# Optimization experiments

Hardware: AMD Instinct MI355X
Metric: run time of the kernel (lower is better)

Reference implementation:

```python
import jax, jax.numpy as jnp
import numpy as np

REPR_IN = (16, 16, 8)
REPR_OUT = (32, 16, 8)
NUM_BASIS = 16
MAX_RADIUS = 2.0
GAMMA = 16.0  # radial basis sharpness

def _dim(repr_):
    return sum(m * (2 * l + 1) for l, m in enumerate(repr_))

DIM_IN = _dim(REPR_IN)          # 104
SIZE_OUT = _dim(REPR_OUT)       # 120
NUM_GATES = sum(REPR_OUT[1:])   # 24
DIM_OUT = SIZE_OUT + NUM_GATES  # 144 (conv emits gates too)


def setup_inputs() -> dict:
    key = jax.random.key(0)
    k1, k2, k3, k4 = jax.random.split(key, 4)
    B, N, M = 4, 1024, 1024
    features = jax.random.normal(k1, (B, DIM_IN, M), jnp.float32)
    difference_matrix = jax.random.normal(k2, (B, N, M, 3), jnp.float32)
    relative_mask = jax.random.uniform(k3, (B, N, M), jnp.float32)
    W = jax.random.normal(k4, (NUM_BASIS, DIM_OUT, DIM_IN), jnp.float32) / np.sqrt(NUM_BASIS * DIM_IN)
    return {"features": features, "difference_matrix": difference_matrix,
            "relative_mask": relative_mask, "W": W}


def _radial_basis(diff):
    # diff: [B, N, M, 3] -> phi: [B, N, M, K]
    r = jnp.sqrt(jnp.sum(diff * diff, axis=-1) + 1e-12)
    centers = jnp.linspace(0.0, MAX_RADIUS, NUM_BASIS, dtype=diff.dtype)
    return jnp.exp(-GAMMA * jnp.square(r[..., None] - centers))


def reference(features, difference_matrix, relative_mask, W):
    # SE3PointConvolution: per-pair kernel K[b,n,m] = sum_k phi_k(|r_nm|) W[k]
    # masked by relative_mask; out[b,o,n] = sum_m K[b,n,m,o,i] feat[b,i,m].
    # Fused so the [B,N,M,144,104] kernel is never materialized.
    phi = _radial_basis(difference_matrix) * relative_mask[..., None]  # [B,N,M,K]
    tmp = jnp.einsum('bnmk,bim->bnki', phi, features)                  # [B,N,K,DIM_IN]
    y = jnp.einsum('bnki,koi->bon', tmp, W)                            # [B,DIM_OUT,N]

    B, _, N = y.shape
    # scalar (l=0) activation, bias=False
    outs = [jax.nn.relu(y[:, :REPR_OUT[0]])]
    # gates: last NUM_GATES channels, sigmoid
    g = jax.nn.sigmoid(y[:, SIZE_OUT:])
    begin_y, begin_g = REPR_OUT[0], 0
    for l, mul in enumerate(REPR_OUT):
        if l == 0 or mul == 0:
            continue
        d = 2 * l + 1
        fy = y[:, begin_y:begin_y + mul * d].reshape(B, mul, d, N)
        fg = g[:, begin_g:begin_g + mul].reshape(B, mul, 1, N)
        outs.append((fy * fg).reshape(B, mul * d, N))
        begin_y += mul * d
        begin_g += mul
    return jnp.concatenate(outs, axis=1)  # [B, SIZE_OUT, N]
```

## Files before the change

### kernel.cpp

```cpp
#include <hip/hip_runtime.h>


typedef __attribute__((ext_vector_type(4))) float f32x4;
typedef __attribute__((ext_vector_type(8))) short s16x8;

#define DI 104
#define DO 144
#define MT 64
#define TTST 1688
#define YST 9

#define W_ELEMS 239616
#define F_ELEMS 425984

#define OFF_PHI0 0
#define OFF_PHI1 16384
#define OFF_FEAT0 32768
#define OFF_FEAT1 47104
#define OFF_Y 61440
#define SMEM_TOTAL (61440 + 144*9*4)

__device__ __forceinline__ float fexp2(float x) {
#if __has_builtin(__builtin_amdgcn_exp2f)
    return __builtin_amdgcn_exp2f(x);
#else
    return exp2f(x);
#endif
}
__device__ __forceinline__ float flog2(float x) {
#if __has_builtin(__builtin_amdgcn_logf)
    return __builtin_amdgcn_logf(x);
#else
    return log2f(x);
#endif
}
__device__ __forceinline__ float fsqrt_(float x) {
#if __has_builtin(__builtin_amdgcn_sqrtf)
    return __builtin_amdgcn_sqrtf(x);
#else
    return sqrtf(x);
#endif
}
__device__ __forceinline__ float frcp_(float x) {
#if __has_builtin(__builtin_amdgcn_rcpf)
    return __builtin_amdgcn_rcpf(x);
#else
    return 1.0f / x;
#endif
}
__device__ __forceinline__ unsigned int pkbf(float lo, float hi) {
    unsigned int a = __builtin_bit_cast(unsigned int, lo) + 0x8000u;
    unsigned int b = __builtin_bit_cast(unsigned int, hi) + 0x8000u;
    return __builtin_amdgcn_perm(b, a, 0x07060302u);
}
__device__ __forceinline__ unsigned short f2b(float f) {
    return (unsigned short)((__builtin_bit_cast(unsigned int, f) + 0x8000u) >> 16);
}

__global__ __launch_bounds__(256, 8)
void cvt_kernel(const float* __restrict__ feat_g, const float* __restrict__ W_g,
                unsigned short* __restrict__ ws)
{
    int gid = blockIdx.x * 256 + threadIdx.x;
    const float* src;
    unsigned short* dst;
    if (gid < W_ELEMS/8) {
        src = W_g + gid*8;  dst = ws + gid*8;
    } else {
        int g2 = gid - W_ELEMS/8;
        src = feat_g + g2*8; dst = ws + W_ELEMS + g2*8;
    }
    f32x4 a = *(const f32x4*)src;
    f32x4 b = *(const f32x4*)(src + 4);
    unsigned int o[4] = { pkbf(a[0],a[1]), pkbf(a[2],a[3]), pkbf(b[0],b[1]), pkbf(b[2],b[3]) };
    *(f32x4*)dst = *(f32x4*)o;
}

__global__ __launch_bounds__(512, 4)
void pgb_kernel(const unsigned short* __restrict__ ws,
                const float* __restrict__ diff_g,
                const float* __restrict__ mask_g,
                float* __restrict__ out_g)
{
    const unsigned short* Wbf    = ws;
    const unsigned short* featbf = ws + W_ELEMS;

    __shared__ __align__(16) unsigned char smem[SMEM_TOTAL];
    unsigned short* Tt   = (unsigned short*)(smem);
    float*          ylds = (float*)(smem + OFF_Y);

    const int t    = threadIdx.x;
    const int b    = blockIdx.x >> 7;
    const int n0   = (blockIdx.x & 127) << 3;
    const int wave = t >> 6;
    const int lane = t & 63;
    const int l15  = lane & 15;
    const int q    = lane >> 4;
    const int wr   = wave >> 1;
    const int ct0  = (wave & 1) << 2;
    const int sw   = l15 & 7;

    if (t < 256) {
        ((unsigned int*)(smem + OFF_FEAT0 + DI*128))[t] = 0u;
        ((unsigned int*)(smem + OFF_FEAT1 + DI*128))[t] = 0u;
    }

    f32x4 acc[2][4];
#pragma unroll
    for (int rr = 0; rr < 2; ++rr)
#pragma unroll
        for (int cc = 0; cc < 4; ++cc)
            acc[rr][cc] = (f32x4){0.f, 0.f, 0.f, 0.f};

    const int pn = t >> 6;
    const int kh = (t >> 5) & 1;
    const int pml = (t & 31) << 1;
    const int pblk = (t & 31) >> 2;
    const int pin  = pml & 7;
    const float CEXP = -23.083120654223414f;
    const float A1   = 6.155498841126244f;
    const float V2   = -0.8207331788168325f;
    const float K0OFF = kh ? 1.0666666666666667f : 0.f;
    const float S0B   = kh ? -6.976232019943076f : -0.41036658940841624f;
    const size_t dmrow = (size_t)((b << 10) + n0 + pn) << 10;

    const int fi0 = t >> 3, fj = t & 7;
    const int fi1 = 64 + (t >> 3);
    const int fjs = (fj ^ (fi0 & 7)) << 3;
    const size_t fbase = (size_t)b * DI << 10;

    float dx0, dy0, dz0, dx1, dy1, dz1, mk0, mk1;
    s16x8 fr0 = {}, fr1 = {};
    {
        const float* dp = diff_g + (dmrow + pml)*3;
        dx0=dp[0]; dy0=dp[1]; dz0=dp[2]; dx1=dp[3]; dy1=dp[4]; dz1=dp[5];
        const float* mp = mask_g + dmrow + pml;
        mk0=mp[0]; mk1=mp[1];
        fr0 = *(const s16x8*)(featbf + fbase + ((size_t)fi0 << 10) + (fj << 3));
        if (t < 320)
            fr1 = *(const s16x8*)(featbf + fbase + ((size_t)fi1 << 10) + (fj << 3));
    }

    for (int s = 0; s < 16; ++s) {
        const int ms = s * MT;
        unsigned short* phibuf  = (unsigned short*)(smem + ((s & 1) ? OFF_PHI1 : OFF_PHI0));
        unsigned short* featbuf = (unsigned short*)(smem + ((s & 1) ? OFF_FEAT1 : OFF_FEAT0));
        {
            float r0 = fsqrt_(fmaf(dx0,dx0, fmaf(dy0,dy0, fmaf(dz0,dz0, 1e-12f))));
            float r1 = fsqrt_(fmaf(dx1,dx1, fmaf(dy1,dy1, fmaf(dz1,dz1, 1e-12f))));
            float t0 = r0 - K0OFF, t1 = r1 - K0OFF;
            float E0 = fmaf(CEXP*t0, t0, flog2(mk0));
            float E1 = fmaf(CEXP*t1, t1, flog2(mk1));
            float s0 = fmaf(A1, r0, S0B);
            float s1 = fmaf(A1, r1, S0B);
            unsigned short* pw = phibuf + (pn*16 + kh*8)*64 + pin;
#pragma unroll
            for (int j = 0; j < 8; ++j) {
                float p0 = fexp2(E0);
                float p1 = fexp2(E1);
                *(unsigned int*)(pw + j*64 + ((pblk ^ j) << 3)) = pkbf(p0, p1);
                E0 += s0; s0 += V2;
                E1 += s1; s1 += V2;
            }
        }
        *(s16x8*)(featbuf + fi0*64 + fjs) = fr0;
        if (t < 320)
            *(s16x8*)(featbuf + fi1*64 + fjs) = fr1;
        __syncthreads();
        if (s < 15) {
            const float* dp = diff_g + (dmrow + ms + MT + pml)*3;
            dx0=dp[0]; dy0=dp[1]; dz0=dp[2]; dx1=dp[3]; dy1=dp[4]; dz1=dp[5];
            const float* mp = mask_g + dmrow + ms + MT + pml;
            mk0=mp[0]; mk1=mp[1];
            fr0 = *(const s16x8*)(featbf + fbase + ((size_t)fi0 << 10) + ms + MT + (fj << 3));
            if (t < 320)
                fr1 = *(const s16x8*)(featbf + fbase + ((size_t)fi1 << 10) + ms + MT + (fj << 3));
        }
#pragma unroll
        for (int kk = 0; kk < 2; ++kk) {
            const int mo = ((kk*4 + q) ^ sw) << 3;
            s16x8 a0 = *(const s16x8*)(phibuf + ((2*wr    )*16 + l15)*64 + mo);
            s16x8 a1 = *(const s16x8*)(phibuf + ((2*wr + 1)*16 + l15)*64 + mo);
#pragma unroll
            for (int cc = 0; cc < 4; ++cc) {
                if (ct0 + cc < 7) {
                    s16x8 bf = *(const s16x8*)(featbuf + ((ct0+cc)*16 + l15)*64 + mo);
                    acc[0][cc] = __builtin_amdgcn_mfma_f32_16x16x32_bf16(a0, bf, acc[0][cc], 0, 0, 0);
                    acc[1][cc] = __builtin_amdgcn_mfma_f32_16x16x32_bf16(a1, bf, acc[1][cc], 0, 0, 0);
                }
            }
        }
    }

    __syncthreads();

#pragma unroll
    for (int rr = 0; rr < 2; ++rr) {
        int nloc = 2*wr + rr;
#pragma unroll
        for (int cc = 0; cc < 4; ++cc) {
            int i = (ct0+cc)*16 + l15;
            if (ct0 + cc < 7 && i < DI) {
#pragma unroll
                for (int r = 0; r < 4; ++r)
                    Tt[nloc*TTST + (q*4+r)*DI + i] = f2b(acc[rr][cc][r]);
            }
        }
    }
    __syncthreads();

    f32x4 y0 = (f32x4){0.f,0.f,0.f,0.f}, y1 = (f32x4){0.f,0.f,0.f,0.f};
    const int o0 = wave*16 + l15;
    const int o1 = 128 + l15;
#pragma unroll 4
    for (int s3 = 0; s3 < 52; ++s3) {
        int a = s3*4 + q;
        int k = a / 13;
        int i = (a - k*13) << 3;
        s16x8 bf = *(const s16x8*)(Tt + (l15 & 7)*TTST + s3*32 + q*8);
        s16x8 af = *(const s16x8*)(Wbf + (size_t)(k*DO + o0)*DI + i);
        y0 = __builtin_amdgcn_mfma_f32_16x16x32_bf16(af, bf, y0, 0, 0, 0);
        if (wave == 0) {
            s16x8 ag = *(const s16x8*)(Wbf + (size_t)(k*DO + o1)*DI + i);
            y1 = __builtin_amdgcn_mfma_f32_16x16x32_bf16(ag, bf, y1, 0, 0, 0);
        }
    }
    if (l15 < 8) {
#pragma unroll
        for (int r = 0; r < 4; ++r)
            ylds[(wave*16 + q*4 + r)*YST + l15] = y0[r];
        if (wave == 0) {
#pragma unroll
            for (int r = 0; r < 4; ++r)
                ylds[(128 + q*4 + r)*YST + l15] = y1[r];
        }
    }
    __syncthreads();

    const float L2E = 1.4426950408889634f;
    for (int idx = t; idx < 120*8; idx += 512) {
        int o = idx >> 3, nn = idx & 7;
        float y = ylds[o*YST + nn];
        float v;
        if (o < 32) {
            v = fmaxf(y, 0.f);
        } else if (o < 80) {
            float g = ylds[(120 + (o-32)/3)*YST + nn];
            v = y * frcp_(1.f + fexp2(-g*L2E));
        } else {
            float g = ylds[(136 + (o-80)/5)*YST + nn];
            v = y * frcp_(1.f + fexp2(-g*L2E));
        }
        out_g[((size_t)(b*120 + o) << 10) + n0 + nn] = v;
    }
}

extern "C" void kernel_launch(void* const* d_in, const int* in_sizes, int n_in,
                              void* d_out, int out_size, void* d_ws, size_t ws_size,
                              hipStream_t stream) {
    const float* feat = (const float*)d_in[0];
    const float* diff = (const float*)d_in[1];
    const float* mask = (const float*)d_in[2];
    const float* W    = (const float*)d_in[3];
    float* out = (float*)d_out;
    unsigned short* ws = (unsigned short*)d_ws;
    (void)in_sizes; (void)n_in; (void)out_size; (void)ws_size;
    cvt_kernel<<<dim3((W_ELEMS + F_ELEMS)/8/256), dim3(256), 0, stream>>>(feat, W, ws);
    pgb_kernel<<<dim3(512), dim3(512), 0, stream>>>(ws, diff, mask, out);
}
```

Baseline: 142.5 us.

## Compute radial basis in registers per wave and feed MFMA directly, drop LDS staging

Each wave now owns one output row n and computes phi for its own 16 basis functions and 8 m-values per lane directly in registers, packing them into the MFMA A operand. Features are loaded straight from global memory into B fragments instead of being staged through double-buffered LDS, which removes the per-step __syncthreads and the phi/feature LDS traffic. The diff/mask loads are vectorized and software-pipelined across half-steps, and the mask is multiplied in linear space instead of folded into the exponent via log2. The trade-off is redundant global feature loads across the 8 waves (relying on cache), more exp evaluations per lane, and higher register pressure.

After: 246.4 us. 1.73x slower.

```diff
diff --git a/kernel.cpp b/kernel.cpp
--- a/kernel.cpp
+++ b/kernel.cpp
@@ -3,35 +3,24 @@
 
 typedef __attribute__((ext_vector_type(4))) float f32x4;
 typedef __attribute__((ext_vector_type(8))) short s16x8;
+typedef __attribute__((ext_vector_type(4))) unsigned int u32x4;
 
 #define DI 104
 #define DO 144
-#define MT 64
 #define TTST 1688
 #define YST 9
 
 #define W_ELEMS 239616
 #define F_ELEMS 425984
 
-#define OFF_PHI0 0
-#define OFF_PHI1 16384
-#define OFF_FEAT0 32768
-#define OFF_FEAT1 47104
-#define OFF_Y 61440
-#define SMEM_TOTAL (61440 + 144*9*4)
+#define OFF_Y 27008
+#define SMEM_TOTAL (27008 + 144*9*4)
 
 __device__ __forceinline__ float fexp2(float x) {
 #if __has_builtin(__builtin_amdgcn_exp2f)
     return __builtin_amdgcn_exp2f(x);
 #else
     return exp2f(x);
-#endif
-}
-__device__ __forceinline__ float flog2(float x) {
-#if __has_builtin(__builtin_amdgcn_logf)
-    return __builtin_amdgcn_logf(x);
-#else
-    return log2f(x);
 #endif
 }
 __device__ __forceinline__ float fsqrt_(float x) {
@@ -86,7 +75,7 @@
     const unsigned short* featbf = ws + W_ELEMS;
 
     __shared__ __align__(16) unsigned char smem[SMEM_TOTAL];
-    unsigned short* Tt   = (unsigned short*)(smem);
+    unsigned short* Tt   = (unsigned short*)smem;
     float*          ylds = (float*)(smem + OFF_Y);
 
     const int t    = threadIdx.x;
@@ -96,115 +85,75 @@
     const int lane = t & 63;
     const int l15  = lane & 15;
     const int q    = lane >> 4;
-    const int wr   = wave >> 1;
-    const int ct0  = (wave & 1) << 2;
-    const int sw   = l15 & 7;
-
-    if (t < 256) {
-        ((unsigned int*)(smem + OFF_FEAT0 + DI*128))[t] = 0u;
-        ((unsigned int*)(smem + OFF_FEAT1 + DI*128))[t] = 0u;
-    }
-
-    f32x4 acc[2][4];
-#pragma unroll
-    for (int rr = 0; rr < 2; ++rr)
-#pragma unroll
-        for (int cc = 0; cc < 4; ++cc)
-            acc[rr][cc] = (f32x4){0.f, 0.f, 0.f, 0.f};
-
-    const int pn = t >> 6;
-    const int kh = (t >> 5) & 1;
-    const int pml = (t & 31) << 1;
-    const int pblk = (t & 31) >> 2;
-    const int pin  = pml & 7;
+    const int mq   = q << 3;
+
     const float CEXP = -23.083120654223414f;
-    const float A1   = 6.155498841126244f;
-    const float V2   = -0.8207331788168325f;
-    const float K0OFF = kh ? 1.0666666666666667f : 0.f;
-    const float S0B   = kh ? -6.976232019943076f : -0.41036658940841624f;
-    const size_t dmrow = (size_t)((b << 10) + n0 + pn) << 10;
-
-    const int fi0 = t >> 3, fj = t & 7;
-    const int fi1 = 64 + (t >> 3);
-    const int fjs = (fj ^ (fi0 & 7)) << 3;
-    const size_t fbase = (size_t)b * DI << 10;
-
-    float dx0, dy0, dz0, dx1, dy1, dz1, mk0, mk1;
-    s16x8 fr0 = {}, fr1 = {};
-    {
-        const float* dp = diff_g + (dmrow + pml)*3;
-        dx0=dp[0]; dy0=dp[1]; dz0=dp[2]; dx1=dp[3]; dy1=dp[4]; dz1=dp[5];
-        const float* mp = mask_g + dmrow + pml;
-        mk0=mp[0]; mk1=mp[1];
-        fr0 = *(const s16x8*)(featbf + fbase + ((size_t)fi0 << 10) + (fj << 3));
-        if (t < 320)
-            fr1 = *(const s16x8*)(featbf + fbase + ((size_t)fi1 << 10) + (fj << 3));
-    }
-
+    const float ck   = (float)l15 * (2.0f/15.0f);
+    const float B1k  = -2.0f * CEXP * ck;
+    const float B0k  = CEXP * ck * ck;
+
+    const size_t drow  = ((size_t)((b << 10) + n0 + wave)) << 10;
+    const size_t fbase = ((size_t)b * DI) << 10;
+
+    f32x4 acc[7];
+#pragma unroll
+    for (int cc = 0; cc < 7; ++cc) acc[cc] = (f32x4){0.f, 0.f, 0.f, 0.f};
+
+    f32x4 D0[6], D1[6], M0[2], M1[2];
+
+    auto loadDM = [&](f32x4* D, f32x4* M, int m0) {
+        const float* dp = diff_g + (drow + m0)*3;
+#pragma unroll
+        for (int u = 0; u < 6; ++u) D[u] = *(const f32x4*)(dp + 4*u);
+        const float* mp = mask_g + drow + m0;
+        M[0] = *(const f32x4*)mp;
+        M[1] = *(const f32x4*)(mp + 4);
+    };
+
+    auto halfstep = [&](const f32x4* D, const f32x4* M, int m0) {
+        s16x8 bfr[7];
+#pragma unroll
+        for (int cc = 0; cc < 6; ++cc) {
+            int i = cc*16 + l15;
+            bfr[cc] = *(const s16x8*)(featbf + fbase + ((size_t)i << 10) + m0);
+        }
+        bfr[6] = *(const s16x8*)(featbf + fbase + ((size_t)(96 + (l15 & 7)) << 10) + m0);
+        if (l15 >= 8) bfr[6] = (s16x8){0,0,0,0,0,0,0,0};
+        float p[8];
+#pragma unroll
+        for (int j = 0; j < 8; ++j) {
+            float dx = D[(3*j+0) >> 2][(3*j+0) & 3];
+            float dy = D[(3*j+1) >> 2][(3*j+1) & 3];
+            float dz = D[(3*j+2) >> 2][(3*j+2) & 3];
+            float r  = fsqrt_(fmaf(dx, dx, fmaf(dy, dy, fmaf(dz, dz, 1e-12f))));
+            float e  = fmaf(r, fmaf(CEXP, r, B1k), B0k);
+            p[j] = fexp2(e) * M[j >> 2][j & 3];
+        }
+        u32x4 pk;
+        pk[0] = pkbf(p[0], p[1]); pk[1] = pkbf(p[2], p[3]);
+        pk[2] = pkbf(p[4], p[5]); pk[3] = pkbf(p[6], p[7]);
+        s16x8 af = __builtin_bit_cast(s16x8, pk);
+#pragma unroll
+        for (int cc = 0; cc < 7; ++cc)
+            acc[cc] = __builtin_amdgcn_mfma_f32_16x16x32_bf16(af, bfr[cc], acc[cc], 0, 0, 0);
+    };
+
+    loadDM(D0, M0, mq);
     for (int s = 0; s < 16; ++s) {
-        const int ms = s * MT;
-        unsigned short* phibuf  = (unsigned short*)(smem + ((s & 1) ? OFF_PHI1 : OFF_PHI0));
-        unsigned short* featbuf = (unsigned short*)(smem + ((s & 1) ? OFF_FEAT1 : OFF_FEAT0));
-        {
-            float r0 = fsqrt_(fmaf(dx0,dx0, fmaf(dy0,dy0, fmaf(dz0,dz0, 1e-12f))));
-            float r1 = fsqrt_(fmaf(dx1,dx1, fmaf(dy1,dy1, fmaf(dz1,dz1, 1e-12f))));
-            float t0 = r0 - K0OFF, t1 = r1 - K0OFF;
-            float E0 = fmaf(CEXP*t0, t0, flog2(mk0));
-            float E1 = fmaf(CEXP*t1, t1, flog2(mk1));
-            float s0 = fmaf(A1, r0, S0B);
-            float s1 = fmaf(A1, r1, S0B);
-            unsigned short* pw = phibuf + (pn*16 + kh*8)*64 + pin;
-#pragma unroll
-            for (int j = 0; j < 8; ++j) {
-                float p0 = fexp2(E0);
-                float p1 = fexp2(E1);
-                *(unsigned int*)(pw + j*64 + ((pblk ^ j) << 3)) = pkbf(p0, p1);
-                E0 += s0; s0 += V2;
-                E1 += s1; s1 += V2;
-            }
-        }
-        *(s16x8*)(featbuf + fi0*64 + fjs) = fr0;
-        if (t < 320)
-            *(s16x8*)(featbuf + fi1*64 + fjs) = fr1;
-        __syncthreads();
-        if (s < 15) {
-            const float* dp = diff_g + (dmrow + ms + MT + pml)*3;
-            dx0=dp[0]; dy0=dp[1]; dz0=dp[2]; dx1=dp[3]; dy1=dp[4]; dz1=dp[5];
-            const float* mp = mask_g + dmrow + ms + MT + pml;
-            mk0=mp[0]; mk1=mp[1];
-            fr0 = *(const s16x8*)(featbf + fbase + ((size_t)fi0 << 10) + ms + MT + (fj << 3));
-            if (t < 320)
-                fr1 = *(const s16x8*)(featbf + fbase + ((size_t)fi1 << 10) + ms + MT + (fj << 3));
-        }
-#pragma unroll
-        for (int kk = 0; kk < 2; ++kk) {
-            const int mo = ((kk*4 + q) ^ sw) << 3;
-            s16x8 a0 = *(const s16x8*)(phibuf + ((2*wr    )*16 + l15)*64 + mo);
-            s16x8 a1 = *(const s16x8*)(phibuf + ((2*wr + 1)*16 + l15)*64 + mo);
-#pragma unroll
-            for (int cc = 0; cc < 4; ++cc) {
-                if (ct0 + cc < 7) {
-                    s16x8 bf = *(const s16x8*)(featbuf + ((ct0+cc)*16 + l15)*64 + mo);
-                    acc[0][cc] = __builtin_amdgcn_mfma_f32_16x16x32_bf16(a0, bf, acc[0][cc], 0, 0, 0);
-                    acc[1][cc] = __builtin_amdgcn_mfma_f32_16x16x32_bf16(a1, bf, acc[1][cc], 0, 0, 0);
-                }
-            }
-        }
-    }
-
-    __syncthreads();
-
-#pragma unroll
-    for (int rr = 0; rr < 2; ++rr) {
-        int nloc = 2*wr + rr;
-#pragma unroll
-        for (int cc = 0; cc < 4; ++cc) {
-            int i = (ct0+cc)*16 + l15;
-            if (ct0 + cc < 7 && i < DI) {
-#pragma unroll
-                for (int r = 0; r < 4; ++r)
-                    Tt[nloc*TTST + (q*4+r)*DI + i] = f2b(acc[rr][cc][r]);
-            }
+        const int m00 = s*64 + mq;
+        loadDM(D1, M1, m00 + 32);
+        halfstep(D0, M0, m00);
+        if (s < 15) loadDM(D0, M0, m00 + 64);
+        halfstep(D1, M1, m00 + 32);
+    }
+
+#pragma unroll
+    for (int cc = 0; cc < 7; ++cc) {
+        int i = cc*16 + l15;
+        if (cc < 6 || l15 < 8) {
+#pragma unroll
+            for (int r = 0; r < 4; ++r)
+                Tt[wave*TTST + (q*4 + r)*DI + i] = f2b(acc[cc][r]);
         }
     }
     __syncthreads();
```

## Software-pipeline phi generation one stage ahead of MFMA GEMM

Applied to the files above, without the earlier changes.

Restructures the main loop so the radial-basis phi tile and feature tile for stage s+1 are computed and written to the alternate LDS buffer while stage s is consumed by MFMA, with global loads prefetched two stages ahead. This leaves one barrier per iteration instead of a compute-then-sync-then-GEMM sequence, letting exp/VALU work overlap matrix work across waves. It adds a prologue and epilogue, keeps more values live in registers (the pk array plus prefetched inputs), and the last iteration reloads stage 15 redundantly.

Measured after the change: 141.5 us. Within noise of the previous version (-0.8%).

```diff
diff --git a/kernel.cpp b/kernel.cpp
--- a/kernel.cpp
+++ b/kernel.cpp
@@ -6,7 +6,6 @@
 
 #define DI 104
 #define DO 144
-#define MT 64
 #define TTST 1688
 #define YST 9
 
@@ -76,6 +75,71 @@
     *(f32x4*)dst = *(f32x4*)o;
 }
 
+#define LOAD_DM(M0)                                                    \
+    do {                                                               \
+        const float* dp_ = diff_g + (dmrow + (M0) + pml)*3;            \
+        dx0 = dp_[0]; dy0 = dp_[1]; dz0 = dp_[2];                      \
+        dx1 = dp_[3]; dy1 = dp_[4]; dz1 = dp_[5];                      \
+        const float* mp_ = mask_g + dmrow + (M0) + pml;                \
+        mk0 = mp_[0]; mk1 = mp_[1];                                    \
+    } while (0)
+
+#define LOAD_FEAT(M0)                                                          \
+    do {                                                                       \
+        fr0 = *(const s16x8*)(featbf + fbase + ((size_t)fi0 << 10) + (M0) + (fj << 3)); \
+        if (t < 320)                                                           \
+            fr1 = *(const s16x8*)(featbf + fbase + ((size_t)fi1 << 10) + (M0) + (fj << 3)); \
+    } while (0)
+
+#define COMPUTE_PHI()                                                  \
+    do {                                                               \
+        float r0_ = fsqrt_(fmaf(dx0,dx0, fmaf(dy0,dy0, fmaf(dz0,dz0, 1e-12f)))); \
+        float r1_ = fsqrt_(fmaf(dx1,dx1, fmaf(dy1,dy1, fmaf(dz1,dz1, 1e-12f)))); \
+        float t0_ = r0_ - K0OFF, t1_ = r1_ - K0OFF;                    \
+        float E0_ = fmaf(CEXP*t0_, t0_, flog2(mk0));                   \
+        float E1_ = fmaf(CEXP*t1_, t1_, flog2(mk1));                   \
+        float s0_ = fmaf(A1, r0_, S0B);                                \
+        float s1_ = fmaf(A1, r1_, S0B);                                \
+        _Pragma("unroll")                                              \
+        for (int j_ = 0; j_ < 8; ++j_) {                               \
+            pk[j_] = pkbf(fexp2(E0_), fexp2(E1_));                     \
+            E0_ += s0_; s0_ += V2;                                     \
+            E1_ += s1_; s1_ += V2;                                     \
+        }                                                              \
+    } while (0)
+
+#define WRITE_PHI(BUF)                                                 \
+    do {                                                               \
+        unsigned short* pw_ = (BUF) + (pn*16 + kh*8)*64 + pin;         \
+        _Pragma("unroll")                                              \
+        for (int j_ = 0; j_ < 8; ++j_)                                 \
+            *(unsigned int*)(pw_ + j_*64 + ((pblk ^ j_) << 3)) = pk[j_]; \
+    } while (0)
+
+#define WRITE_FEAT(BUF)                                                \
+    do {                                                               \
+        *(s16x8*)((BUF) + fi0*64 + fjs) = fr0;                         \
+        if (t < 320) *(s16x8*)((BUF) + fi1*64 + fjs) = fr1;            \
+    } while (0)
+
+#define GEMM1(PBUF, FBUF)                                              \
+    do {                                                               \
+        _Pragma("unroll")                                              \
+        for (int kk_ = 0; kk_ < 2; ++kk_) {                            \
+            const int mo_ = ((kk_*4 + q) ^ sw) << 3;                   \
+            s16x8 a0_ = *(const s16x8*)((PBUF) + ((2*wr    )*16 + l15)*64 + mo_); \
+            s16x8 a1_ = *(const s16x8*)((PBUF) + ((2*wr + 1)*16 + l15)*64 + mo_); \
+            _Pragma("unroll")                                          \
+            for (int cc_ = 0; cc_ < 4; ++cc_) {                        \
+                if (ct0 + cc_ < 7) {                                   \
+                    s16x8 bf_ = *(const s16x8*)((FBUF) + ((ct0+cc_)*16 + l15)*64 + mo_); \
+                    acc[0][cc_] = __builtin_amdgcn_mfma_f32_16x16x32_bf16(a0_, bf_, acc[0][cc_], 0, 0, 0); \
+                    acc[1][cc_] = __builtin_amdgcn_mfma_f32_16x16x32_bf16(a1_, bf_, acc[1][cc_], 0, 0, 0); \
+                }                                                      \
+            }                                                          \
+        }                                                              \
+    } while (0)
+
 __global__ __launch_bounds__(512, 4)
 void pgb_kernel(const unsigned short* __restrict__ ws,
                 const float* __restrict__ diff_g,
@@ -86,8 +150,12 @@
     const unsigned short* featbf = ws + W_ELEMS;
 
     __shared__ __align__(16) unsigned char smem[SMEM_TOTAL];
-    unsigned short* Tt   = (unsigned short*)(smem);
+    unsigned short* Tt   = (unsigned short*)smem;
     float*          ylds = (float*)(smem + OFF_Y);
+    unsigned short* phi0b  = (unsigned short*)(smem + OFF_PHI0);
+    unsigned short* phi1b  = (unsigned short*)(smem + OFF_PHI1);
+    unsigned short* feat0b = (unsigned short*)(smem + OFF_FEAT0);
+    unsigned short* feat1b = (unsigned short*)(smem + OFF_FEAT1);
 
     const int t    = threadIdx.x;
     const int b    = blockIdx.x >> 7;
@@ -112,9 +180,9 @@
         for (int cc = 0; cc < 4; ++cc)
             acc[rr][cc] = (f32x4){0.f, 0.f, 0.f, 0.f};
 
-    const int pn = t >> 6;
-    const int kh = (t >> 5) & 1;
-    const int pml = (t & 31) << 1;
+    const int pn   = t >> 6;
+    const int kh   = (t >> 5) & 1;
+    const int pml  = (t & 31) << 1;
     const int pblk = (t & 31) >> 2;
     const int pin  = pml & 7;
     const float CEXP = -23.083120654223414f;
@@ -131,66 +199,34 @@
 
     float dx0, dy0, dz0, dx1, dy1, dz1, mk0, mk1;
     s16x8 fr0 = {}, fr1 = {};
-    {
-        const float* dp = diff_g + (dmrow + pml)*3;
-        dx0=dp[0]; dy0=dp[1]; dz0=dp[2]; dx1=dp[3]; dy1=dp[4]; dz1=dp[5];
-        const float* mp = mask_g + dmrow + pml;
-        mk0=mp[0]; mk1=mp[1];
-        fr0 = *(const s16x8*)(featbf + fbase + ((size_t)fi0 << 10) + (fj << 3));
-        if (t < 320)
-            fr1 = *(const s16x8*)(featbf + fbase + ((size_t)fi1 << 10) + (fj << 3));
-    }
-
-    for (int s = 0; s < 16; ++s) {
-        const int ms = s * MT;
-        unsigned short* phibuf  = (unsigned short*)(smem + ((s & 1) ? OFF_PHI1 : OFF_PHI0));
-        unsigned short* featbuf = (unsigned short*)(smem + ((s & 1) ? OFF_FEAT1 : OFF_FEAT0));
+    unsigned int pk[8];
+
+    LOAD_DM(0);
+    LOAD_FEAT(0);
+    COMPUTE_PHI();
+    WRITE_PHI(phi0b);
+    WRITE_FEAT(feat0b);
+    LOAD_DM(64);
+    LOAD_FEAT(64);
+
+    for (int s = 0; s < 15; ++s) {
+        unsigned short* rp = (s & 1) ? phi1b  : phi0b;
+        unsigned short* rf = (s & 1) ? feat1b : feat0b;
+        unsigned short* wp = (s & 1) ? phi0b  : phi1b;
+        unsigned short* wf = (s & 1) ? feat0b : feat1b;
+        __syncthreads();
+        COMPUTE_PHI();
+        WRITE_PHI(wp);
+        WRITE_FEAT(wf);
         {
-            float r0 = fsqrt_(fmaf(dx0,dx0, fmaf(dy0,dy0, fmaf(dz0,dz0, 1e-12f))));
-            float r1 = fsqrt_(fmaf(dx1,dx1, fmaf(dy1,dy1, fmaf(dz1,dz1, 1e-12f))));
-            float t0 = r0 - K0OFF, t1 = r1 - K0OFF;
-            float E0 = fmaf(CEXP*t0, t0, flog2(mk0));
-            float E1 = fmaf(CEXP*t1, t1, flog2(mk1));
-            float s0 = fmaf(A1, r0, S0B);
-            float s1 = fmaf(A1, r1, S0B);
-            unsigned short* pw = phibuf + (pn*16 + kh*8)*64 + pin;
-#pragma unroll
-            for (int j = 0; j < 8; ++j) {
-                float p0 = fexp2(E0);
-                float p1 = fexp2(E1);
-                *(unsigned int*)(pw + j*64 + ((pblk ^ j) << 3)) = pkbf(p0, p1);
-                E0 += s0; s0 += V2;
-                E1 += s1; s1 += V2;
-            }
-        }
-        *(s16x8*)(featbuf + fi0*64 + fjs) = fr0;
-        if (t < 320)
-            *(s16x8*)(featbuf + fi1*64 + fjs) = fr1;
-        __syncthreads();
-        if (s < 15) {
-            const float* dp = diff_g + (dmrow + ms + MT + pml)*3;
-            dx0=dp[0]; dy0=dp[1]; dz0=dp[2]; dx1=dp[3]; dy1=dp[4]; dz1=dp[5];
-            const float* mp = mask_g + dmrow + ms + MT + pml;
-            mk0=mp[0]; mk1=mp[1];
-            fr0 = *(const s16x8*)(featbf + fbase + ((size_t)fi0 << 10) + ms + MT + (fj << 3));
-            if (t < 320)
-                fr1 = *(const s16x8*)(featbf + fbase + ((size_t)fi1 << 10) + ms + MT + (fj << 3));
-        }
-#pragma unroll
-        for (int kk = 0; kk < 2; ++kk) {
-            const int mo = ((kk*4 + q) ^ sw) << 3;
-            s16x8 a0 = *(const s16x8*)(phibuf + ((2*wr    )*16 + l15)*64 + mo);
-            s16x8 a1 = *(const s16x8*)(phibuf + ((2*wr + 1)*16 + l15)*64 + mo);
-#pragma unroll
-            for (int cc = 0; cc < 4; ++cc) {
-                if (ct0 + cc < 7) {
-                    s16x8 bf = *(const s16x8*)(featbuf + ((ct0+cc)*16 + l15)*64 + mo);
-                    acc[0][cc] = __builtin_amdgcn_mfma_f32_16x16x32_bf16(a0, bf, acc[0][cc], 0, 0, 0);
-                    acc[1][cc] = __builtin_amdgcn_mfma_f32_16x16x32_bf16(a1, bf, acc[1][cc], 0, 0, 0);
-                }
-            }
-        }
-    }
+            const int mnext = (s < 14 ? (s + 2) : 15) * 64;
+            LOAD_DM(mnext);
+            LOAD_FEAT(mnext);
+        }
+        GEMM1(rp, rf);
+    }
+    __syncthreads();
+    GEMM1(phi1b, feat1b);
 
     __syncthreads();
 
```
